# Performance work log

Measured on AMD Instinct MI355X. Metric: run time of the kernel, lower is better.

The kernel has to match this reference:

```python
import jax, jax.numpy as jnp
import numpy as np

ORDER = 8
ALPHA = 1.0
BETA = 1.0
IN_SIZE = 512
OUT_SIZE = 512
BATCH = 4096


def jacobi_values(x, order, a, b):
    """x: [B, I] raw input. Returns Jacobi polynomial values [B, I, order+1]."""
    x = jnp.tanh(x)
    vals = [jnp.ones_like(x), 0.5 * (a + b + 2) * x - 0.5 * (a - b)]
    for i in range(2, order + 1):
        k1 = (2 * i + a + b) * (2 * i + a + b - 1) / (2 * i * (i + a + b))
        k2 = (2 * i + a + b - 1) * (a * a - b * b) / (2 * i * (i + a + b) * (2 * i + a + b - 2))
        k3 = (i + a - 1) * (i + b - 1) * (2 * i + a + b) / (i * (i + a + b) * (2 * i + a + b - 2))
        vals.append((k1 * x + k2) * vals[-1] - k3 * vals[-2])
    return jnp.stack(vals, axis=-1)


def setup_inputs() -> dict:
    key = jax.random.key(0)
    kx, kw, kc = jax.random.split(key, 3)
    x = jax.random.normal(kx, (BATCH, IN_SIZE), dtype=jnp.float32)
    weights = jax.random.normal(kw, (OUT_SIZE, IN_SIZE), dtype=jnp.float32)
    # coefficients: one (order+1)-vector per (output, input) pair, init ~ N(0,1)*0.1
    coeff = jax.random.normal(kc, (OUT_SIZE, IN_SIZE, ORDER + 1), dtype=jnp.float32) * 0.1
    return {"x": x, "weights": weights, "coeff": coeff}


def reference(x, weights, coeff):
    # J: [B, I, K] with K = order+1
    J = jacobi_values(x, ORDER, ALPHA, BETA)
    # transformed_x[b,o,i] = sum_k coeff[o,i,k] * J[b,i,k]
    # output[b,o] = sum_i transformed_x[b,o,i] * weights[o,i]
    return jnp.einsum('bik,oik,oi->bo', J, coeff, weights)
```

## Files before the change

kernel.cpp:

```cpp
#include <hip/hip_runtime.h>
#include <hip/hip_bf16.h>

constexpr int BATCH = 4096;
constexpr int IN    = 512;
constexpr int OUT   = 512;
constexpr int ORD   = 8;
constexpr int NK    = ORD + 1;
constexpr float FA  = 1.0f, FB = 1.0f;

constexpr int KP     = IN * ORD;
constexpr int KS_TOT = KP / 32;

typedef __attribute__((ext_vector_type(8))) short short8;
typedef __attribute__((ext_vector_type(4))) float floatx4;

#define AS1 __attribute__((address_space(1)))
#define AS3 __attribute__((address_space(3)))

__device__ __forceinline__ float bf16bits_to_f32(short s) {
    union { unsigned int u; float f; } cv;
    cv.u = ((unsigned int)(unsigned short)s) << 16;
    return cv.f;
}
__device__ __forceinline__ short f32_to_bf16bits(float f) {
    __hip_bfloat16 h = __float2bfloat16(f);
    return *(short*)&h;
}

__global__ __launch_bounds__(256) void prep(const float* __restrict__ x,
                                            const float* __restrict__ w,
                                            const float* __restrict__ coeff,
                                            short* __restrict__ A2,
                                            short* __restrict__ B2,
                                            float* __restrict__ bias) {
    const int bid  = blockIdx.x;
    const int tid  = threadIdx.x;
    const int lane = tid & 63;
    const int quad = lane >> 4;
    const int l15  = lane & 15;

    if (bid < 1024) {
        const int mt  = bid >> 2;
        const int sub = ((bid & 3) << 2) + (tid >> 6);
        const int b   = mt * 16 + l15;
        const int i0  = sub * 32 + quad * 8;
        const float* xr = x + (size_t)b * IN + i0;
        float t[8];
#pragma unroll
        for (int e = 0; e < 8; ++e) {
            float xc = fminf(fmaxf(xr[e], -9.0f), 9.0f);
            float ex = __expf(2.0f * xc);
            t[e] = (ex - 1.0f) / (ex + 1.0f);
        }
        float pp[8], pc[8];
#pragma unroll
        for (int e = 0; e < 8; ++e) {
            pp[e] = 1.0f;
            pc[e] = 0.5f * (FA + FB + 2.0f) * t[e] - 0.5f * (FA - FB);
        }
        {
            short8 v;
#pragma unroll
            for (int e = 0; e < 8; ++e) v[e] = f32_to_bf16bits(pc[e]);
            *(short8*)(A2 + (((size_t)mt * KS_TOT + sub) * 64 + lane) * 8) = v;
        }
#pragma unroll
        for (int n = 2; n <= ORD; ++n) {
            float fn = (float)n;
            float k1 = (2.f*fn+FA+FB)*(2.f*fn+FA+FB-1.f) / (2.f*fn*(fn+FA+FB));
            float k2 = (2.f*fn+FA+FB-1.f)*(FA*FA-FB*FB) /
                       (2.f*fn*(fn+FA+FB)*(2.f*fn+FA+FB-2.f));
            float k3 = (fn+FA-1.f)*(fn+FB-1.f)*(2.f*fn+FA+FB) /
                       (fn*(fn+FA+FB)*(2.f*fn+FA+FB-2.f));
            short8 v;
#pragma unroll
            for (int e = 0; e < 8; ++e) {
                float nx = (k1*t[e] + k2)*pc[e] - k3*pp[e];
                pp[e] = pc[e]; pc[e] = nx;
                v[e] = f32_to_bf16bits(nx);
            }
            const int ks = (n - 1) * 16 + sub;
            *(short8*)(A2 + (((size_t)mt * KS_TOT + ks) * 64 + lane) * 8) = v;
        }
    } else if (bid < 1152) {
        const int b2  = bid - 1024;
        const int nt  = b2 >> 2;
        const int sub = ((b2 & 3) << 2) + (tid >> 6);
        const int o   = nt * 16 + l15;
        const int i0  = sub * 32 + quad * 8;
        const float* wr = w + (size_t)o * IN + i0;
        float wv[8];
#pragma unroll
        for (int e = 0; e < 8; ++e) wv[e] = wr[e];
        const float* cf = coeff + ((size_t)o * IN + i0) * NK;
#pragma unroll
        for (int n = 1; n <= ORD; ++n) {
            short8 v;
#pragma unroll
            for (int e = 0; e < 8; ++e)
                v[e] = f32_to_bf16bits(cf[(size_t)e * NK + n] * wv[e]);
            const int ks = (n - 1) * 16 + sub;
            *(short8*)(B2 + (((size_t)nt * KS_TOT + ks) * 64 + lane) * 8) = v;
        }
    } else {
        const int bb = bid - 1152;
        const int o  = bb * 4 + (tid >> 6);
        const float* cf = coeff + (size_t)o * IN * NK;
        const float* wr = w + (size_t)o * IN;
        float acc = 0.0f;
#pragma unroll
        for (int r = 0; r < IN / 64; ++r) {
            int i = r * 64 + lane;
            acc = fmaf(cf[(size_t)i * NK], wr[i], acc);
        }
#pragma unroll
        for (int off = 32; off >= 1; off >>= 1)
            acc += __shfl_xor(acc, off, 64);
        if (lane == 0) bias[o] = acc;
    }
}

__global__ __launch_bounds__(256) void gemm_full(
        const short* __restrict__ A2,
        const short* __restrict__ B2,
        const float* __restrict__ bias,
        float* __restrict__ out)
{
    __shared__ short sA[4 * 8192];

    const int tid  = threadIdx.x;
    const int lane = tid & 63;
    const int quad = lane >> 4;
    const int l15  = lane & 15;
    const int wave = tid >> 6;
    const int mw   = wave & 1;
    const int nw   = wave >> 1;
    const int bx = blockIdx.x;
    const int by = blockIdx.y;

    const short* pb[2];
#pragma unroll
    for (int j = 0; j < 2; ++j)
        pb[j] = B2 + (((size_t)(by * 4 + nw * 2 + j) * KS_TOT) * 64 + lane) * 8;

    const int wv = wave;
    const short* aBase = A2 + ((size_t)(bx * 8) * KS_TOT) * 512;

#define STAGE2(BT, BUF)                                                      \
    _Pragma("unroll")                                                        \
    for (int c = 0; c < 4; ++c) {                                            \
        const int ll = c * 4 + wv;                                           \
        const int mt = ll & 7;                                               \
        const int s  = ll >> 3;                                              \
        __builtin_amdgcn_global_load_lds(                                    \
            (const AS1 unsigned int*)(aBase +                                \
                ((size_t)mt * KS_TOT + (BT) * 2 + s) * 512 + lane * 8),      \
            (AS3 unsigned int*)(sA + (BUF) * 8192 + (c * 256 + tid) * 8),    \
            16, 0, 0);                                                       \
    }

#define BLOAD(S0, S1, K0)                                                    \
    _Pragma("unroll")                                                        \
    for (int j = 0; j < 2; ++j) {                                            \
        S0[j] = *(const short8*)(pb[j] + (size_t)(K0) * 512);                \
        S1[j] = *(const short8*)(pb[j] + (size_t)((K0) + 1) * 512);          \
    }

    floatx4 acc[4][2];
#pragma unroll
    for (int i = 0; i < 4; ++i)
#pragma unroll
        for (int j = 0; j < 2; ++j) acc[i][j] = (floatx4)0.0f;

#define ASTEP(BUFI, S, BSLOT)                                                \
    {                                                                        \
        short8 af[4];                                                        \
        _Pragma("unroll")                                                    \
        for (int i = 0; i < 4; ++i)                                          \
            af[i] = *(const short8*)(sA + (BUFI) * 8192 +                    \
                        (((S) * 8 + mw * 4 + i) * 64 + lane) * 8);           \
        __builtin_amdgcn_s_setprio(1);                                       \
        _Pragma("unroll")                                                    \
        for (int i = 0; i < 4; ++i)                                          \
            _Pragma("unroll")                                                \
            for (int j = 0; j < 2; ++j)                                      \
                acc[i][j] = __builtin_amdgcn_mfma_f32_16x16x32_bf16(         \
                                af[i], BSLOT[j], acc[i][j], 0, 0, 0);        \
        __builtin_amdgcn_s_setprio(0);                                       \
    }

    short8 bsA0[2], bsA1[2], bsB0[2], bsB1[2];

    STAGE2(0, 0)
    BLOAD(bsA0, bsA1, 0)
    STAGE2(1, 1)
    STAGE2(2, 2)
    asm volatile("s_waitcnt vmcnt(12)" ::: "memory");
    __builtin_amdgcn_s_barrier();

#define ITERX(T, BUFI, SBUF, C0, C1, L0, L1)                                 \
    BLOAD(L0, L1, 2 * (T) + 2)                                               \
    STAGE2((T) + 3, SBUF)                                                    \
    ASTEP(BUFI, 0, C0) ASTEP(BUFI, 1, C1)                                    \
    asm volatile("s_waitcnt vmcnt(12)" ::: "memory");                        \
    __builtin_amdgcn_s_barrier();

    for (int q = 0; q < 15; ++q) {
        const int t0 = q * 4;
        ITERX(t0,     0, 3, bsA0, bsA1, bsB0, bsB1)
        ITERX(t0 + 1, 1, 0, bsB0, bsB1, bsA0, bsA1)
        ITERX(t0 + 2, 2, 1, bsA0, bsA1, bsB0, bsB1)
        ITERX(t0 + 3, 3, 2, bsB0, bsB1, bsA0, bsA1)
    }
    ITERX(60, 0, 3, bsA0, bsA1, bsB0, bsB1)
    BLOAD(bsA0, bsA1, 124)
    ASTEP(1, 0, bsB0) ASTEP(1, 1, bsB1)
    asm volatile("s_waitcnt vmcnt(8)" ::: "memory");
    __builtin_amdgcn_s_barrier();
    BLOAD(bsB0, bsB1, 126)
    ASTEP(2, 0, bsA0) ASTEP(2, 1, bsA1)
    asm volatile("s_waitcnt vmcnt(4)" ::: "memory");
    __builtin_amdgcn_s_barrier();
    ASTEP(3, 0, bsB0) ASTEP(3, 1, bsB1)

#undef ITERX
#undef ASTEP
#undef BLOAD
#undef STAGE2

    const int m0 = bx * 128, n0 = by * 64;
    float bj[2];
#pragma unroll
    for (int j = 0; j < 2; ++j) bj[j] = bias[n0 + nw * 32 + j * 16 + l15];
#pragma unroll
    for (int i = 0; i < 4; ++i) {
        const int r0 = m0 + mw * 64 + i * 16 + quad * 4;
#pragma unroll
        for (int j = 0; j < 2; ++j) {
            const int c = n0 + nw * 32 + j * 16 + l15;
#pragma unroll
            for (int r = 0; r < 4; ++r)
                out[(size_t)(r0 + r) * OUT + c] = acc[i][j][r] + bj[j];
        }
    }
}

extern "C" void kernel_launch(void* const* d_in, const int* in_sizes, int n_in,
                              void* d_out, int out_size, void* d_ws, size_t ws_size,
                              hipStream_t stream) {
    const float* x     = (const float*)d_in[0];
    const float* w     = (const float*)d_in[1];
    const float* coeff = (const float*)d_in[2];
    float* out = (float*)d_out;

    char* ws = (char*)d_ws;
    short* A2 = (short*)ws;
    char* p1c = ws + (size_t)BATCH * KP * 2;
    short* B2 = (short*)p1c;
    float* bias = (float*)(p1c + (size_t)OUT * KP * 2);

    prep<<<1280, 256, 0, stream>>>(x, w, coeff, A2, B2, bias);
    gemm_full<<<dim3(32, 8), 256, 0, stream>>>(A2, B2, bias, out);
}
```

Before: 111.6 us.

## Halve GEMM N-tile, use triple-buffered LDS and two blocks per CU

The GEMM tile shrinks from 128x64 to 128x32, so each wave handles one N sub-tile and the grid doubles to 32x16 blocks. The A staging buffer goes from four LDS stages to three, and launch bounds now ask for two blocks per CU. The goal is more blocks and better occupancy to fill the GPU's CUs, which were underused at 256 blocks. In exchange, A-tile reuse per block is halved, so A traffic from global/L2 doubles, and the prefetch depth is shallower.

```diff
diff --git a/kernel.cpp b/kernel.cpp
--- a/kernel.cpp
+++ b/kernel.cpp
@@ -120,13 +120,13 @@
     }
 }
 
-__global__ __launch_bounds__(256) void gemm_full(
+__global__ __launch_bounds__(256, 2) void gemm_full(
         const short* __restrict__ A2,
         const short* __restrict__ B2,
         const float* __restrict__ bias,
         float* __restrict__ out)
 {
-    __shared__ short sA[4 * 8192];
+    __shared__ short sA[3 * 8192];
 
     const int tid  = threadIdx.x;
     const int lane = tid & 63;
@@ -138,10 +138,7 @@
     const int bx = blockIdx.x;
     const int by = blockIdx.y;
 
-    const short* pb[2];
-#pragma unroll
-    for (int j = 0; j < 2; ++j)
-        pb[j] = B2 + (((size_t)(by * 4 + nw * 2 + j) * KS_TOT) * 64 + lane) * 8;
+    const short* pb = B2 + ((size_t)(by * 2 + nw) * KS_TOT * 64 + lane) * 8;
 
     const int wv = wave;
     const short* aBase = A2 + ((size_t)(bx * 8) * KS_TOT) * 512;
@@ -160,17 +157,14 @@
     }
 
 #define BLOAD(S0, S1, K0)                                                    \
-    _Pragma("unroll")                                                        \
-    for (int j = 0; j < 2; ++j) {                                            \
-        S0[j] = *(const short8*)(pb[j] + (size_t)(K0) * 512);                \
-        S1[j] = *(const short8*)(pb[j] + (size_t)((K0) + 1) * 512);          \
-    }
-
-    floatx4 acc[4][2];
-#pragma unroll
-    for (int i = 0; i < 4; ++i)
-#pragma unroll
-        for (int j = 0; j < 2; ++j) acc[i][j] = (floatx4)0.0f;
+    {                                                                        \
+        S0 = *(const short8*)(pb + (size_t)(K0) * 512);                      \
+        S1 = *(const short8*)(pb + (size_t)((K0) + 1) * 512);                \
+    }
+
+    floatx4 acc[4];
+#pragma unroll
+    for (int i = 0; i < 4; ++i) acc[i] = (floatx4)0.0f;
 
 #define ASTEP(BUFI, S, BSLOT)                                                \
     {                                                                        \
@@ -182,66 +176,57 @@
         __builtin_amdgcn_s_setprio(1);                                       \
         _Pragma("unroll")                                                    \
         for (int i = 0; i < 4; ++i)                                          \
-            _Pragma("unroll")                                                \
-            for (int j = 0; j < 2; ++j)                                      \
-                acc[i][j] = __builtin_amdgcn_mfma_f32_16x16x32_bf16(         \
-                                af[i], BSLOT[j], acc[i][j], 0, 0, 0);        \
+            acc[i] = __builtin_amdgcn_mfma_f32_16x16x32_bf16(                \
+                         af[i], BSLOT, acc[i], 0, 0, 0);                     \
         __builtin_amdgcn_s_setprio(0);                                       \
     }
 
-    short8 bsA0[2], bsA1[2], bsB0[2], bsB1[2];
+    short8 bsA0, bsA1, bsB0, bsB1;
 
     STAGE2(0, 0)
+    STAGE2(1, 1)
     BLOAD(bsA0, bsA1, 0)
-    STAGE2(1, 1)
-    STAGE2(2, 2)
-    asm volatile("s_waitcnt vmcnt(12)" ::: "memory");
+    asm volatile("s_waitcnt vmcnt(10)" ::: "memory");
     __builtin_amdgcn_s_barrier();
 
-#define ITERX(T, BUFI, SBUF, C0, C1, L0, L1)                                 \
-    BLOAD(L0, L1, 2 * (T) + 2)                                               \
-    STAGE2((T) + 3, SBUF)                                                    \
-    ASTEP(BUFI, 0, C0) ASTEP(BUFI, 1, C1)                                    \
-    asm volatile("s_waitcnt vmcnt(12)" ::: "memory");                        \
+#define ITERX(T, BUF, SBUF, C0, C1, N0, N1)                                  \
+    STAGE2((T) + 2, SBUF)                                                    \
+    BLOAD(N0, N1, 2 * (T) + 2)                                               \
+    ASTEP(BUF, 0, C0) ASTEP(BUF, 1, C1)                                      \
+    asm volatile("s_waitcnt vmcnt(10)" ::: "memory");                        \
     __builtin_amdgcn_s_barrier();
 
-    for (int q = 0; q < 15; ++q) {
-        const int t0 = q * 4;
-        ITERX(t0,     0, 3, bsA0, bsA1, bsB0, bsB1)
+    for (int g = 0; g < 10; ++g) {
+        const int t0 = g * 6;
+        ITERX(t0,     0, 2, bsA0, bsA1, bsB0, bsB1)
         ITERX(t0 + 1, 1, 0, bsB0, bsB1, bsA0, bsA1)
         ITERX(t0 + 2, 2, 1, bsA0, bsA1, bsB0, bsB1)
-        ITERX(t0 + 3, 3, 2, bsB0, bsB1, bsA0, bsA1)
-    }
-    ITERX(60, 0, 3, bsA0, bsA1, bsB0, bsB1)
-    BLOAD(bsA0, bsA1, 124)
-    ASTEP(1, 0, bsB0) ASTEP(1, 1, bsB1)
-    asm volatile("s_waitcnt vmcnt(8)" ::: "memory");
-    __builtin_amdgcn_s_barrier();
+        ITERX(t0 + 3, 0, 2, bsB0, bsB1, bsA0, bsA1)
+        ITERX(t0 + 4, 1, 0, bsA0, bsA1, bsB0, bsB1)
+        ITERX(t0 + 5, 2, 1, bsB0, bsB1, bsA0, bsA1)
+    }
+    ITERX(60, 0, 2, bsA0, bsA1, bsB0, bsB1)
+    ITERX(61, 1, 0, bsB0, bsB1, bsA0, bsA1)
     BLOAD(bsB0, bsB1, 126)
     ASTEP(2, 0, bsA0) ASTEP(2, 1, bsA1)
-    asm volatile("s_waitcnt vmcnt(4)" ::: "memory");
+    asm volatile("s_waitcnt vmcnt(2)" ::: "memory");
     __builtin_amdgcn_s_barrier();
-    ASTEP(3, 0, bsB0) ASTEP(3, 1, bsB1)
+    ASTEP(0, 0, bsB0) ASTEP(0, 1, bsB1)
 
 #undef ITERX
 #undef ASTEP
 #undef BLOAD
 #undef STAGE2
 
-    const int m0 = bx * 128, n0 = by * 64;
-    float bj[2];
-#pragma unroll
-    for (int j = 0; j < 2; ++j) bj[j] = bias[n0 + nw * 32 + j * 16 + l15];
+    const int m0 = bx * 128, n0 = by * 32;
+    const int c  = n0 + nw * 16 + l15;
+    const float bj = bias[c];
 #pragma unroll
     for (int i = 0; i < 4; ++i) {
         const int r0 = m0 + mw * 64 + i * 16 + quad * 4;
 #pragma unroll
-        for (int j = 0; j < 2; ++j) {
-            const int c = n0 + nw * 32 + j * 16 + l15;
-#pragma unroll
-            for (int r = 0; r < 4; ++r)
-                out[(size_t)(r0 + r) * OUT + c] = acc[i][j][r] + bj[j];
-        }
+        for (int r = 0; r < 4; ++r)
+            out[(size_t)(r0 + r) * OUT + c] = acc[i][r] + bj;
     }
 }
 
@@ -260,5 +245,5 @@
     float* bias = (float*)(p1c + (size_t)OUT * KP * 2);
 
     prep<<<1280, 256, 0, stream>>>(x, w, coeff, A2, B2, bias);
-    gemm_full<<<dim3(32, 8), 256, 0, stream>>>(A2, B2, bias, out);
-}
+    gemm_full<<<dim3(32, 16), 256, 0, stream>>>(A2, B2, bias, out);
+}
```

Result: faster. 109.2 us, median of 2 (-2.1%).
